# Kernel optimization log

Measured on AMD Instinct MI355X. Metric: run time of the kernel, lower is better.

## Reference

```python
import jax, jax.numpy as jnp
import numpy as np
import math

B, S, H, NH, HD, RD, INNER, MAXPOS, EPS = 2, 2048, 4096, 16, 256, 64, 16384, 2048, 1e-5


def setup_inputs() -> dict:
    key = jax.random.key(0)
    ks = jax.random.split(key, 8)
    sd = 0.02
    return {
        "hidden_states": jax.random.normal(ks[0], (B, S, H), jnp.float32),
        "attention_mask": jnp.ones((B, S), jnp.int32),
        "position_ids": jnp.broadcast_to(jnp.arange(S, dtype=jnp.int32), (B, S)),
        "ln_scale": jnp.ones((H,), jnp.float32),
        "ln_bias": jnp.zeros((H,), jnp.float32),
        "wq": jax.random.normal(ks[1], (H, H), jnp.float32) * sd,
        "wk": jax.random.normal(ks[2], (H, H), jnp.float32) * sd,
        "wv": jax.random.normal(ks[3], (H, H), jnp.float32) * sd,
        "wo": jax.random.normal(ks[4], (H, H), jnp.float32) * sd,
        "w_in": jax.random.normal(ks[5], (H, INNER), jnp.float32) * sd,
        "b_in": jnp.zeros((INNER,), jnp.float32),
        "w_out": jax.random.normal(ks[6], (INNER, H), jnp.float32) * sd,
        "b_out": jnp.zeros((H,), jnp.float32),
    }


def _rotate_every_two(t):
    # interleave (-odd, even) pairs along last dim
    r = jnp.stack((-t[..., 1::2], t[..., ::2]), axis=-1)
    return r.reshape(t.shape)


def reference(hidden_states, attention_mask, position_ids, ln_scale, ln_bias,
              wq, wk, wv, wo, w_in, b_in, w_out, b_out):
    x = hidden_states
    # LayerNorm (single ln feeds both attn and mlp in GPT-J parallel block)
    mu = jnp.mean(x, axis=-1, keepdims=True)
    var = jnp.mean(jnp.square(x - mu), axis=-1, keepdims=True)
    h = (x - mu) * jax.lax.rsqrt(var + EPS) * ln_scale + ln_bias

    # QKV projections (no bias), split heads: [B,S,NH,HD]
    q = (h @ wq).reshape(B, S, NH, HD)
    k = (h @ wk).reshape(B, S, NH, HD)
    v = (h @ wv).reshape(B, S, NH, HD)

    # sinusoidal table over rotary_dim, gathered by position_ids
    pos = jnp.arange(MAXPOS, dtype=jnp.float32)
    inv_freq = 1.0 / (10000.0 ** (jnp.arange(0, RD, 2, dtype=jnp.float32) / RD))
    freqs = pos[:, None] * inv_freq[None, :]          # [MAXPOS, RD//2]
    table = jnp.concatenate([jnp.sin(freqs), jnp.cos(freqs)], axis=-1)  # [MAXPOS, RD]
    sincos = table[position_ids]                      # [B,S,RD]
    sin, cos = jnp.split(sincos, 2, axis=-1)          # each [B,S,RD//2]
    sinr = jnp.repeat(sin[:, :, None, :], 2, axis=3)  # [B,S,1,RD]
    cosr = jnp.repeat(cos[:, :, None, :], 2, axis=3)

    def rope(t):
        return t * cosr + _rotate_every_two(t) * sinr

    q = jnp.concatenate([rope(q[..., :RD]), q[..., RD:]], axis=-1)
    k = jnp.concatenate([rope(k[..., :RD]), k[..., RD:]], axis=-1)

    # combined causal + padding mask -> additive bias
    causal = jnp.tril(jnp.ones((S, S), dtype=bool))
    mask = (attention_mask[:, None, None, :] > 0) & causal[None, None, :, :]
    bias = jnp.where(mask, 0.0, jnp.finfo(jnp.float32).min)  # [B,1,S,S]

    scale = 1.0 / math.sqrt(HD)
    scores = jnp.einsum('bqhd,bkhd->bhqk', q, k) * scale + bias
    attn = jax.nn.softmax(scores, axis=-1)
    ctx = jnp.einsum('bhqk,bkhd->bqhd', attn, v).reshape(B, S, H)
    attn_out = ctx @ wo

    # MLP on the same LN output (parallel residual), gelu_new ~ tanh gelu
    mlp = jax.nn.gelu(h @ w_in + b_in, approximate=True) @ w_out + b_out

    return x + attn_out + mlp
```

## Files before the change

### kernel.cpp

```cpp
#include <hip/hip_runtime.h>
#include <hip/hip_bf16.h>
#include <math.h>

namespace {

constexpr int kB = 2;
constexpr int kS = 2048;
constexpr int kH = 4096;
constexpr int kNH = 16;
constexpr int kHD = 256;

typedef __attribute__((ext_vector_type(4))) float f32x4;
typedef __attribute__((ext_vector_type(8))) short bf16x8;

__device__ __forceinline__ unsigned short f2bf(float f) {
  unsigned int u = __float_as_uint(f);
  u += 0x7FFFu + ((u >> 16) & 1u);
  return (unsigned short)(u >> 16);
}
__device__ __forceinline__ float bf2f(unsigned short h) {
  return __uint_as_float(((unsigned int)h) << 16);
}
__device__ __forceinline__ void gl2lds16(const void* g, void* l) {
  __builtin_amdgcn_global_load_lds(
      (const __attribute__((address_space(1))) unsigned int*)g,
      (__attribute__((address_space(3))) unsigned int*)l, 16, 0, 0);
}

#define SBAR asm volatile("s_barrier" ::: "memory")
#define LGKM0 asm volatile("s_waitcnt lgkmcnt(0)" ::: "memory")

__global__ __launch_bounds__(256) void ln_fwd(
    const float* __restrict__ x, const float* __restrict__ gam,
    const float* __restrict__ bet, unsigned short* __restrict__ hout,
    float* __restrict__ outp) {
  int row = blockIdx.x;
  int t = threadIdx.x;
  const float4* xr = (const float4*)(x + (size_t)row * kH);
  float4 v[4];
  float sum = 0.f, sq = 0.f;
#pragma unroll
  for (int i = 0; i < 4; i++) {
    v[i] = xr[t + i * 256];
    sum += v[i].x + v[i].y + v[i].z + v[i].w;
    sq += v[i].x * v[i].x + v[i].y * v[i].y + v[i].z * v[i].z + v[i].w * v[i].w;
  }
#pragma unroll
  for (int o = 32; o > 0; o >>= 1) {
    sum += __shfl_xor(sum, o);
    sq += __shfl_xor(sq, o);
  }
  __shared__ float red[8];
  if ((t & 63) == 0) { red[t >> 6] = sum; red[4 + (t >> 6)] = sq; }
  __syncthreads();
  sum = red[0] + red[1] + red[2] + red[3];
  sq = red[4] + red[5] + red[6] + red[7];
  float mu = sum * (1.f / kH);
  float rstd = rsqrtf(sq * (1.f / kH) - mu * mu + 1e-5f);
  const float4* gp = (const float4*)gam;
  const float4* bp = (const float4*)bet;
  ushort4* hr = (ushort4*)(hout + (size_t)row * kH);
  float4* orow = (float4*)(outp + (size_t)row * kH);
#pragma unroll
  for (int i = 0; i < 4; i++) {
    float4 g = gp[t + i * 256];
    float4 bb = bp[t + i * 256];
    ushort4 hv;
    hv.x = f2bf((v[i].x - mu) * rstd * g.x + bb.x);
    hv.y = f2bf((v[i].y - mu) * rstd * g.y + bb.y);
    hv.z = f2bf((v[i].z - mu) * rstd * g.z + bb.z);
    hv.w = f2bf((v[i].w - mu) * rstd * g.w + bb.w);
    hr[t + i * 256] = hv;
    orow[t + i * 256] = v[i];
  }
}

__global__ __launch_bounds__(256) void cvt_t(
    const float* __restrict__ in, int ldin, unsigned short* __restrict__ outp,
    int ldout) {
  __shared__ float tile[32][33];
  int n0 = blockIdx.x * 32, k0 = blockIdx.y * 32;
  int tx = threadIdx.x, ty = threadIdx.y;
#pragma unroll
  for (int i = 0; i < 4; i++)
    tile[ty + i * 8][tx] = in[(size_t)(k0 + ty + i * 8) * ldin + n0 + tx];
  __syncthreads();
#pragma unroll
  for (int i = 0; i < 4; i++)
    outp[(size_t)(n0 + ty + i * 8) * ldout + k0 + tx] =
        f2bf(tile[tx][ty + i * 8]);
}

__global__ __launch_bounds__(256) void vtrans(
    const unsigned short* __restrict__ v, unsigned short* __restrict__ vt) {
  __shared__ unsigned short tile[32][33];
  int bh = blockIdx.z;
  int s0 = blockIdx.x * 32, d0 = blockIdx.y * 32;
  int tx = threadIdx.x, ty = threadIdx.y;
  int b = bh >> 4, h = bh & 15;
  const unsigned short* src = v + (size_t)(b * kS) * kH + h * kHD;
#pragma unroll
  for (int i = 0; i < 4; i++)
    tile[ty + i * 8][tx] = src[(size_t)(s0 + ty + i * 8) * kH + d0 + tx];
  __syncthreads();
  unsigned short* dst = vt + (size_t)bh * kHD * kS;
#pragma unroll
  for (int i = 0; i < 4; i++)
    dst[(size_t)(d0 + ty + i * 8) * kS + s0 + tx] = tile[tx][ty + i * 8];
}

__global__ __launch_bounds__(256) void rope_scale(
    unsigned short* __restrict__ q, unsigned short* __restrict__ k,
    const int* __restrict__ pos) {
  int idx = blockIdx.x * 256 + threadIdx.x;
  int j = idx & 127;
  int rowh = idx >> 7;
  int h = rowh & 15;
  int s = (rowh >> 4) & 2047;
  int b = rowh >> 15;
  size_t off = ((size_t)(b * kS + s)) * kH + h * kHD + 2 * j;
  const float SCALE = 0.0625f;
  if (j < 32) {
    int p = pos[b * kS + s];
    float inv = exp2f(-(float)j * (13.287712379549449f / 32.f));
    float fr = (float)p * inv;
    float sn, cs;
    sincosf(fr, &sn, &cs);
    float e = bf2f(q[off]), o = bf2f(q[off + 1]);
    q[off] = f2bf((e * cs - o * sn) * SCALE);
    q[off + 1] = f2bf((o * cs + e * sn) * SCALE);
    e = bf2f(k[off]); o = bf2f(k[off + 1]);
    k[off] = f2bf(e * cs - o * sn);
    k[off + 1] = f2bf(o * cs + e * sn);
  } else {
    q[off] = f2bf(bf2f(q[off]) * SCALE);
    q[off + 1] = f2bf(bf2f(q[off + 1]) * SCALE);
  }
}

template <int EPI>
__global__ __launch_bounds__(512, 4) void gemmk(
    const unsigned short* __restrict__ A, int lda,
    const unsigned short* __restrict__ Bt, int ldb, void* __restrict__ Cp,
    int ldc, const float* __restrict__ bias, int K, int gx) {
  __shared__ __align__(16) char lds[73728];
  const int t = threadIdx.x;
  const int lane = t & 63, w = t >> 6;
  const int wm = w >> 1, wn = w & 1;
  const int l15 = lane & 15, l4 = lane >> 4;

  const int nwg = gridDim.x;
  const int orig = blockIdx.x;
  const int wg = (orig & 7) * (nwg >> 3) + (orig >> 3);
  const int bx = wg % gx, by = wg / gx;
  const int m0 = by * 256, n0 = bx * 128;

  const int lr = t >> 2, ch = t & 3;
  const int swo = ((ch ^ ((lr & 3) ^ ((lr >> 2) & 3))) << 3);
  const unsigned short* aS0 = A + (size_t)(m0 + lr) * lda + swo;
  const unsigned short* aS1 = A + (size_t)(m0 + 128 + lr) * lda + swo;
  const unsigned short* bS = Bt + (size_t)(n0 + lr) * ldb + swo;
  const int t16 = t * 16;

  const int keyR = (l15 & 3) ^ ((l15 >> 2) & 3);
  const int rch = ((l4 ^ keyR) << 4);
  const int abase = wm * 4096 + l15 * 64 + rch;
  const int bbase = 16384 + wn * 4096 + l15 * 64 + rch;

  f32x4 acc[4][4];
#pragma unroll
  for (int m = 0; m < 4; m++)
#pragma unroll
    for (int n = 0; n < 4; n++) acc[m][n] = (f32x4)(0.f);

  gl2lds16(aS0, lds + t16);
  gl2lds16(aS1, lds + 8192 + t16);
  gl2lds16(bS, lds + 16384 + t16);
  aS0 += 32; aS1 += 32; bS += 32;
  gl2lds16(aS0, lds + 24576 + t16);
  gl2lds16(aS1, lds + 24576 + 8192 + t16);
  gl2lds16(bS, lds + 24576 + 16384 + t16);
  aS0 += 32; aS1 += 32; bS += 32;
  asm volatile("s_waitcnt vmcnt(3)" ::: "memory");
  SBAR;

  int offR = 0, off1 = 24576, offW = 49152;
  const int nt = K >> 5;
  for (int kt = 0; kt < nt; ++kt) {
    if (kt + 2 < nt) {
      gl2lds16(aS0, lds + offW + t16);
      gl2lds16(aS1, lds + offW + 8192 + t16);
      gl2lds16(bS, lds + offW + 16384 + t16);
      aS0 += 32; aS1 += 32; bS += 32;
    }
    const char* cur = lds + offR;
    bf16x8 af[4], bv[4];
#pragma unroll
    for (int m = 0; m < 4; m++)
      af[m] = *(const bf16x8*)(cur + abase + m * 1024);
#pragma unroll
    for (int n = 0; n < 4; n++)
      bv[n] = *(const bf16x8*)(cur + bbase + n * 1024);
    __builtin_amdgcn_s_setprio(1);
#pragma unroll
    for (int m = 0; m < 4; m++)
#pragma unroll
      for (int n = 0; n < 4; n++)
        acc[m][n] = __builtin_amdgcn_mfma_f32_16x16x32_bf16(af[m], bv[n],
                                                            acc[m][n], 0, 0, 0);
    __builtin_amdgcn_s_setprio(0);
    LGKM0;
    if (kt + 2 < nt) asm volatile("s_waitcnt vmcnt(3)" ::: "memory");
    else             asm volatile("s_waitcnt vmcnt(0)" ::: "memory");
    SBAR;
    int tmp = offR; offR = off1; off1 = offW; offW = tmp;
  }

  const int crow = m0 + wm * 64 + l4 * 4;
  const int ccol = n0 + wn * 64 + l15;
#pragma unroll
  for (int m = 0; m < 4; m++) {
#pragma unroll
    for (int n = 0; n < 4; n++) {
      int col = ccol + n * 16;
#pragma unroll
      for (int r = 0; r < 4; r++) {
        int row = crow + m * 16 + r;
        float v = acc[m][n][r];
        size_t idx = (size_t)row * ldc + col;
        if constexpr (EPI == 0) {
          ((unsigned short*)Cp)[idx] = f2bf(v);
        } else if constexpr (EPI == 1) {
          float u = v + bias[col];
          float c = 0.7978845608028654f * (u + 0.044715f * u * u * u);
          float g = u / (1.0f + __expf(-2.0f * c));
          ((unsigned short*)Cp)[idx] = f2bf(g);
        } else if constexpr (EPI == 2) {
          ((float*)Cp)[idx] += v;
        } else {
          ((float*)Cp)[idx] += v + bias[col];
        }
      }
    }
  }
}

__global__ __launch_bounds__(512) void attn_fwd(
    const unsigned short* __restrict__ q, const unsigned short* __restrict__ k,
    const unsigned short* __restrict__ vt, const int* __restrict__ amask,
    unsigned short* __restrict__ ctx) {
  __shared__ __align__(16) char alds[147456];
  const int t = threadIdx.x, lane = t & 63, w = t >> 6;
  const int bid = blockIdx.x;
  const int qb = 15 - (bid >> 5);
  const int bh = bid & 31;
  const int b = bh >> 4, h = bh & 15;
  const int l15 = lane & 15, l4 = lane >> 4;
  const int qbase = qb * 128;

  bf16x8 qf[8];
  {
    int qrow = qbase + w * 16 + l15;
    const unsigned short* qp =
        q + (size_t)(b * kS + qrow) * kH + h * kHD + l4 * 8;
#pragma unroll
    for (int ks = 0; ks < 8; ks++) qf[ks] = *(const bf16x8*)(qp + ks * 32);
  }
  f32x4 o[16];
#pragma unroll
  for (int nf = 0; nf < 16; nf++) o[nf] = (f32x4)(0.f);
  float mr[4] = {-INFINITY, -INFINITY, -INFINITY, -INFINITY};
  float lr[4] = {0.f, 0.f, 0.f, 0.f};

  const unsigned short* kbase = k + (size_t)(b * kS) * kH + h * kHD;
  const unsigned short* vbase = vt + (size_t)bh * kHD * kS;
  unsigned short* sPw = (unsigned short*)(alds + 131072 + w * 2048);
  const int nt = 2 * qb + 2;

  const int krow = t >> 5, kch = t & 31;
  const int kcs = (kch ^ (krow & 7)) * 8;
  const int vrow = t >> 3, vch = t & 7;
  const int vcs = (vch ^ (vrow & 7)) * 8;
  const int t16b = t * 16;

#define ATTN_STAGE(KV0, BUF)                                                 \
  {                                                                          \
    char* kd = alds + (BUF) * 32768;                                         \
    char* vd = alds + 65536 + (BUF) * 32768;                                 \
    _Pragma("unroll") for (int i = 0; i < 4; i++) {                          \
      gl2lds16(kbase + (size_t)((KV0) + krow + i * 16) * kH + kcs,           \
               kd + i * 8192 + t16b);                                        \
      gl2lds16(vbase + (size_t)(vrow + i * 64) * kS + (KV0) + vcs,           \
               vd + i * 8192 + t16b);                                        \
    }                                                                        \
  }

  ATTN_STAGE(0, 0)

  for (int kvt = 0; kvt < nt; kvt++) {
    const int kv0 = kvt * 64;
    const int cb = kvt & 1;
    if (kvt + 1 < nt) {
      ATTN_STAGE(kv0 + 64, cb ^ 1)
      asm volatile("s_waitcnt vmcnt(8)" ::: "memory");
    } else {
      asm volatile("s_waitcnt vmcnt(0)" ::: "memory");
    }
    asm volatile("s_barrier" ::: "memory");

    const unsigned short* sK = (const unsigned short*)(alds + cb * 32768);
    const unsigned short* sV =
        (const unsigned short*)(alds + 65536 + cb * 32768);

    f32x4 sc[4];
#pragma unroll
    for (int g = 0; g < 4; g++) sc[g] = (f32x4)(0.f);
    __builtin_amdgcn_s_setprio(1);
#pragma unroll
    for (int g = 0; g < 4; g++) {
      int row = g * 16 + l15;
#pragma unroll
      for (int ks = 0; ks < 8; ks++) {
        bf16x8 kf =
            *(const bf16x8*)&sK[row * 256 + (((ks * 4 + l4) ^ (row & 7)) * 8)];
        sc[g] = __builtin_amdgcn_mfma_f32_16x16x32_bf16(qf[ks], kf, sc[g], 0, 0, 0);
      }
    }
    __builtin_amdgcn_s_setprio(0);

    int am[4];
#pragma unroll
    for (int g = 0; g < 4; g++) am[g] = amask[b * kS + kv0 + g * 16 + l15];
    float mx[4];
#pragma unroll
    for (int r = 0; r < 4; r++) {
      int qi = qbase + w * 16 + l4 * 4 + r;
      float a = -INFINITY;
#pragma unroll
      for (int g = 0; g < 4; g++) {
        bool ok = (kv0 + g * 16 + l15 <= qi) && (am[g] != 0);
        float s = ok ? sc[g][r] : -INFINITY;
        sc[g][r] = s;
        a = fmaxf(a, s);
      }
#pragma unroll
      for (int d = 1; d < 16; d <<= 1) a = fmaxf(a, __shfl_xor(a, d));
      mx[r] = a;
    }
    bool nd = false;
#pragma unroll
    for (int r = 0; r < 4; r++) nd |= (mx[r] > mr[r] + 8.f);
    if (__any(nd)) {
#pragma unroll
      for (int r = 0; r < 4; r++) {
        float nm = fmaxf(mr[r], mx[r]);
        float c = __expf(mr[r] - nm);
        lr[r] *= c;
        mr[r] = nm;
#pragma unroll
        for (int nf = 0; nf < 16; nf++) o[nf][r] *= c;
      }
    }
#pragma unroll
    for (int r = 0; r < 4; r++) {
      int prow = l4 * 4 + r;
      int pkey = (prow ^ (prow >> 2)) & 7;
      float rs = 0.f;
#pragma unroll
      for (int g = 0; g < 4; g++) {
        float p = __expf(sc[g][r] - mr[r]);
        rs += p;
        int kvl = g * 16 + l15;
        sPw[prow * 64 + (((kvl >> 3) ^ pkey) << 3) + (kvl & 7)] = f2bf(p);
      }
#pragma unroll
      for (int d = 1; d < 16; d <<= 1) rs += __shfl_xor(rs, d);
      lr[r] += rs;
    }
    asm volatile("s_waitcnt lgkmcnt(0)" ::: "memory");

    int rkey = (l15 ^ (l15 >> 2)) & 7;
    bf16x8 pa[2];
#pragma unroll
    for (int ks2 = 0; ks2 < 2; ks2++)
      pa[ks2] = *(const bf16x8*)&sPw[l15 * 64 + (((ks2 * 4 + l4) ^ rkey) << 3)];
    __builtin_amdgcn_s_setprio(1);
#pragma unroll
    for (int nf = 0; nf < 16; nf++) {
      int vr = nf * 16 + l15;
#pragma unroll
      for (int ks2 = 0; ks2 < 2; ks2++) {
        bf16x8 vf =
            *(const bf16x8*)&sV[vr * 64 + (((ks2 * 4 + l4) ^ (vr & 7)) * 8)];
        o[nf] = __builtin_amdgcn_mfma_f32_16x16x32_bf16(pa[ks2], vf, o[nf], 0, 0, 0);
      }
    }
    __builtin_amdgcn_s_setprio(0);
    asm volatile("s_barrier" ::: "memory");
  }

  float invl[4];
#pragma unroll
  for (int r = 0; r < 4; r++) invl[r] = 1.0f / lr[r];
#pragma unroll
  for (int nf = 0; nf < 16; nf++) {
    int d = nf * 16 + l15;
#pragma unroll
    for (int r = 0; r < 4; r++) {
      int qi = qbase + w * 16 + l4 * 4 + r;
      ctx[(size_t)(b * kS + qi) * kH + h * kHD + d] = f2bf(o[nf][r] * invl[r]);
    }
  }
#undef ATTN_STAGE
}

}

extern "C" void kernel_launch(void* const* d_in, const int* in_sizes, int n_in,
                              void* d_out, int out_size, void* d_ws,
                              size_t ws_size, hipStream_t stream) {
  const float* x = (const float*)d_in[0];
  const int* amask = (const int*)d_in[1];
  const int* pos = (const int*)d_in[2];
  const float* lns = (const float*)d_in[3];
  const float* lnb = (const float*)d_in[4];
  const float* wq = (const float*)d_in[5];
  const float* wk = (const float*)d_in[6];
  const float* wv = (const float*)d_in[7];
  const float* wo = (const float*)d_in[8];
  const float* w_in = (const float*)d_in[9];
  const float* b_in = (const float*)d_in[10];
  const float* w_out = (const float*)d_in[11];
  const float* b_out = (const float*)d_in[12];
  float* out = (float*)d_out;

  if (ws_size < 268435456ull) return;
  char* ws = (char*)d_ws;
  unsigned short* h_bf = (unsigned short*)ws;
  unsigned short* big = (unsigned short*)(ws + 33554432ull);
  unsigned short* vbuf = (unsigned short*)(ws + 167772160ull);
  unsigned short* wbuf = (unsigned short*)(ws + 201326592ull);
  unsigned short* mid = big;
  unsigned short* qbuf = big;
  unsigned short* kbuf = big + 16777216;
  unsigned short* vtb = big + 33554432;
  unsigned short* ctxb = vbuf;

  dim3 t256(256);
  dim3 t512(512);
  dim3 t32x8(32, 8);

  ln_fwd<<<kB * kS, t256, 0, stream>>>(x, lns, lnb, h_bf, out);

  for (int c = 0; c < 2; c++) {
    cvt_t<<<dim3(256, 128), t32x8, 0, stream>>>(w_in + c * 8192, 16384, wbuf, 4096);
    gemmk<1><<<dim3(1024), t512, 0, stream>>>(
        h_bf, 4096, wbuf, 4096, mid + c * 8192, 16384, b_in + c * 8192, 4096, 64);
  }
  for (int c = 0; c < 2; c++) {
    cvt_t<<<dim3(128, 256), t32x8, 0, stream>>>(
        w_out + (size_t)c * 8192 * 4096, 4096, wbuf, 8192);
    if (c == 0)
      gemmk<3><<<dim3(512), t512, 0, stream>>>(mid + c * 8192, 16384, wbuf,
                                               8192, out, 4096, b_out, 8192, 32);
    else
      gemmk<2><<<dim3(512), t512, 0, stream>>>(
          mid + c * 8192, 16384, wbuf, 8192, out, 4096, nullptr, 8192, 32);
  }

  const float* wqkv[3] = {wq, wk, wv};
  unsigned short* qkvp[3] = {qbuf, kbuf, vbuf};
  for (int i = 0; i < 3; i++) {
    cvt_t<<<dim3(128, 128), t32x8, 0, stream>>>(wqkv[i], 4096, wbuf, 4096);
    gemmk<0><<<dim3(512), t512, 0, stream>>>(h_bf, 4096, wbuf, 4096,
                                             qkvp[i], 4096, nullptr, 4096, 32);
  }
  rope_scale<<<32768, t256, 0, stream>>>(qbuf, kbuf, pos);
  vtrans<<<dim3(64, 8, 32), t32x8, 0, stream>>>(vbuf, vtb);
  attn_fwd<<<dim3(512), t512, 0, stream>>>(qbuf, kbuf, vtb, amask, ctxb);
  cvt_t<<<dim3(128, 128), t32x8, 0, stream>>>(wo, 4096, wbuf, 4096);
  gemmk<2><<<dim3(512), t512, 0, stream>>>(ctxb, 4096, wbuf, 4096, out,
                                           4096, nullptr, 4096, 32);
}
```

Measured before the change: 2.342 ms.

## Replace GEMM with 256x256-tile kernel using LDS flag sync and 4-stage ring

Swaps the 256x128-tile, triple-buffered GEMM for a 256x256-tile kernel. Each of its 8 waves computes an 8x4 grid of MFMA tiles. Workgroup s_barriers are replaced by per-wave progress flags in LDS: waves spin with s_sleep until every wave has finished loading the current k-slice, over a 4-slot LDS ring with a new swizzle. The aim is more data reuse per tile and less barrier stall. The cost is doubled accumulator registers, lower occupancy (launch bounds 2), and spin-wait overhead and ordering risk.

```diff
diff --git a/kernel.cpp b/kernel.cpp
--- a/kernel.cpp
+++ b/kernel.cpp
@@ -26,9 +26,6 @@
       (const __attribute__((address_space(1))) unsigned int*)g,
       (__attribute__((address_space(3))) unsigned int*)l, 16, 0, 0);
 }
-
-#define SBAR asm volatile("s_barrier" ::: "memory")
-#define LGKM0 asm volatile("s_waitcnt lgkmcnt(0)" ::: "memory")
 
 __global__ __launch_bounds__(256) void ln_fwd(
     const float* __restrict__ x, const float* __restrict__ gam,
@@ -139,87 +136,103 @@
 }
 
 template <int EPI>
-__global__ __launch_bounds__(512, 4) void gemmk(
+__global__ __launch_bounds__(512, 2) void gemmpc(
     const unsigned short* __restrict__ A, int lda,
     const unsigned short* __restrict__ Bt, int ldb, void* __restrict__ Cp,
     int ldc, const float* __restrict__ bias, int K, int gx) {
-  __shared__ __align__(16) char lds[73728];
+  __shared__ __align__(16) char lds[131072 + 32];
+  volatile unsigned* fl = (volatile unsigned*)(lds + 131072);
   const int t = threadIdx.x;
   const int lane = t & 63, w = t >> 6;
-  const int wm = w >> 1, wn = w & 1;
+  const int wm = w >> 2, wn = w & 3;
   const int l15 = lane & 15, l4 = lane >> 4;
 
   const int nwg = gridDim.x;
   const int orig = blockIdx.x;
   const int wg = (orig & 7) * (nwg >> 3) + (orig >> 3);
   const int bx = wg % gx, by = wg / gx;
-  const int m0 = by * 256, n0 = bx * 128;
-
-  const int lr = t >> 2, ch = t & 3;
-  const int swo = ((ch ^ ((lr & 3) ^ ((lr >> 2) & 3))) << 3);
-  const unsigned short* aS0 = A + (size_t)(m0 + lr) * lda + swo;
-  const unsigned short* aS1 = A + (size_t)(m0 + 128 + lr) * lda + swo;
-  const unsigned short* bS = Bt + (size_t)(n0 + lr) * ldb + swo;
-  const int t16 = t * 16;
-
-  const int keyR = (l15 & 3) ^ ((l15 >> 2) & 3);
-  const int rch = ((l4 ^ keyR) << 4);
-  const int abase = wm * 4096 + l15 * 64 + rch;
-  const int bbase = 16384 + wn * 4096 + l15 * 64 + rch;
-
-  f32x4 acc[4][4];
-#pragma unroll
-  for (int m = 0; m < 4; m++)
+  const int m0 = by * 256, n0 = bx * 256;
+
+  const unsigned short* sp[4];
+#pragma unroll
+  for (int i = 0; i < 4; i++) {
+    int g = w * 256 + i * 64 + lane;
+    int gin = g & 1023;
+    int p = gin >> 3, s = (gin & 7) ^ (p & 7);
+    int row = 2 * p + (s >> 2), chunk = s & 3;
+    sp[i] = (g < 1024 ? A + (size_t)(m0 + row) * lda
+                      : Bt + (size_t)(n0 + row) * ldb) + chunk * 8;
+  }
+  const int dstoff = w * 4096 + lane * 16;
+
+  const int swz = ((((l15 & 1) << 2) | l4) ^ ((l15 >> 1) & 7)) << 4;
+  const int abase = wm * 8192 + ((l15 >> 1) << 7) + swz;
+  const int bbase = 16384 + wn * 4096 + ((l15 >> 1) << 7) + swz;
+
+  f32x4 acc[8][4];
+#pragma unroll
+  for (int m = 0; m < 8; m++)
 #pragma unroll
     for (int n = 0; n < 4; n++) acc[m][n] = (f32x4)(0.f);
 
-  gl2lds16(aS0, lds + t16);
-  gl2lds16(aS1, lds + 8192 + t16);
-  gl2lds16(bS, lds + 16384 + t16);
-  aS0 += 32; aS1 += 32; bS += 32;
-  gl2lds16(aS0, lds + 24576 + t16);
-  gl2lds16(aS1, lds + 24576 + 8192 + t16);
-  gl2lds16(bS, lds + 24576 + 16384 + t16);
-  aS0 += 32; aS1 += 32; bS += 32;
-  asm volatile("s_waitcnt vmcnt(3)" ::: "memory");
-  SBAR;
-
-  int offR = 0, off1 = 24576, offW = 49152;
+  if (lane == 0) fl[w] = 0;
+  __syncthreads();
+  {
+    char* dst = lds + dstoff;
+#pragma unroll
+    for (int i = 0; i < 4; i++) gl2lds16(sp[i], dst + i * 1024);
+#pragma unroll
+    for (int i = 0; i < 4; i++) sp[i] += 32;
+  }
+
   const int nt = K >> 5;
   for (int kt = 0; kt < nt; ++kt) {
-    if (kt + 2 < nt) {
-      gl2lds16(aS0, lds + offW + t16);
-      gl2lds16(aS1, lds + offW + 8192 + t16);
-      gl2lds16(bS, lds + offW + 16384 + t16);
-      aS0 += 32; aS1 += 32; bS += 32;
-    }
-    const char* cur = lds + offR;
-    bf16x8 af[4], bv[4];
-#pragma unroll
-    for (int m = 0; m < 4; m++)
+    if (kt + 1 < nt) {
+      char* dst = lds + ((kt + 1) & 3) * 32768 + dstoff;
+#pragma unroll
+      for (int i = 0; i < 4; i++) gl2lds16(sp[i], dst + i * 1024);
+#pragma unroll
+      for (int i = 0; i < 4; i++) sp[i] += 32;
+      asm volatile("s_waitcnt vmcnt(4)" ::: "memory");
+    } else {
+      asm volatile("s_waitcnt vmcnt(0)" ::: "memory");
+    }
+    if (lane == 0) fl[w] = (unsigned)(kt + 1);
+    {
+      int spins = 0;
+      while (spins < (1 << 22)) {
+        unsigned v = fl[lane & 7];
+        v = min(v, (unsigned)__shfl_xor((int)v, 1));
+        v = min(v, (unsigned)__shfl_xor((int)v, 2));
+        v = min(v, (unsigned)__shfl_xor((int)v, 4));
+        if (v >= (unsigned)(kt + 1)) break;
+        __builtin_amdgcn_s_sleep(1);
+        ++spins;
+      }
+    }
+    __builtin_amdgcn_sched_barrier(0);
+    const char* cur = lds + (kt & 3) * 32768;
+    bf16x8 af[8], bv[4];
+#pragma unroll
+    for (int m = 0; m < 8; m++)
       af[m] = *(const bf16x8*)(cur + abase + m * 1024);
 #pragma unroll
     for (int n = 0; n < 4; n++)
       bv[n] = *(const bf16x8*)(cur + bbase + n * 1024);
     __builtin_amdgcn_s_setprio(1);
 #pragma unroll
-    for (int m = 0; m < 4; m++)
+    for (int m = 0; m < 8; m++)
 #pragma unroll
       for (int n = 0; n < 4; n++)
         acc[m][n] = __builtin_amdgcn_mfma_f32_16x16x32_bf16(af[m], bv[n],
                                                             acc[m][n], 0, 0, 0);
     __builtin_amdgcn_s_setprio(0);
-    LGKM0;
-    if (kt + 2 < nt) asm volatile("s_waitcnt vmcnt(3)" ::: "memory");
-    else             asm volatile("s_waitcnt vmcnt(0)" ::: "memory");
-    SBAR;
-    int tmp = offR; offR = off1; off1 = offW; offW = tmp;
-  }
-
-  const int crow = m0 + wm * 64 + l4 * 4;
+  }
+
+  const int crow = m0 + wm * 128 + l4 * 4;
   const int ccol = n0 + wn * 64 + l15;
 #pragma unroll
-  for (int m = 0; m < 4; m++) {
+  for (int m = 0; m < 8; m++) {
 #pragma unroll
     for (int n = 0; n < 4; n++) {
       int col = ccol + n * 16;
@@ -454,31 +467,31 @@
 
   for (int c = 0; c < 2; c++) {
     cvt_t<<<dim3(256, 128), t32x8, 0, stream>>>(w_in + c * 8192, 16384, wbuf, 4096);
-    gemmk<1><<<dim3(1024), t512, 0, stream>>>(
-        h_bf, 4096, wbuf, 4096, mid + c * 8192, 16384, b_in + c * 8192, 4096, 64);
+    gemmpc<1><<<dim3(512), t512, 0, stream>>>(
+        h_bf, 4096, wbuf, 4096, mid + c * 8192, 16384, b_in + c * 8192, 4096, 32);
   }
   for (int c = 0; c < 2; c++) {
     cvt_t<<<dim3(128, 256), t32x8, 0, stream>>>(
         w_out + (size_t)c * 8192 * 4096, 4096, wbuf, 8192);
     if (c == 0)
-      gemmk<3><<<dim3(512), t512, 0, stream>>>(mid + c * 8192, 16384, wbuf,
-                                               8192, out, 4096, b_out, 8192, 32);
+      gemmpc<3><<<dim3(256), t512, 0, stream>>>(mid + c * 8192, 16384, wbuf,
+                                                8192, out, 4096, b_out, 8192, 16);
     else
-      gemmk<2><<<dim3(512), t512, 0, stream>>>(
-          mid + c * 8192, 16384, wbuf, 8192, out, 4096, nullptr, 8192, 32);
+      gemmpc<2><<<dim3(256), t512, 0, stream>>>(
+          mid + c * 8192, 16384, wbuf, 8192, out, 4096, nullptr, 8192, 16);
   }
 
   const float* wqkv[3] = {wq, wk, wv};
   unsigned short* qkvp[3] = {qbuf, kbuf, vbuf};
   for (int i = 0; i < 3; i++) {
     cvt_t<<<dim3(128, 128), t32x8, 0, stream>>>(wqkv[i], 4096, wbuf, 4096);
-    gemmk<0><<<dim3(512), t512, 0, stream>>>(h_bf, 4096, wbuf, 4096,
-                                             qkvp[i], 4096, nullptr, 4096, 32);
+    gemmpc<0><<<dim3(256), t512, 0, stream>>>(h_bf, 4096, wbuf, 4096,
+                                              qkvp[i], 4096, nullptr, 4096, 16);
   }
   rope_scale<<<32768, t256, 0, stream>>>(qbuf, kbuf, pos);
   vtrans<<<dim3(64, 8, 32), t32x8, 0, stream>>>(vbuf, vtb);
   attn_fwd<<<dim3(512), t512, 0, stream>>>(qbuf, kbuf, vtb, amask, ctxb);
   cvt_t<<<dim3(128, 128), t32x8, 0, stream>>>(wo, 4096, wbuf, 4096);
-  gemmk<2><<<dim3(512), t512, 0, stream>>>(ctxb, 4096, wbuf, 4096, out,
-                                           4096, nullptr, 4096, 32);
-}
+  gemmpc<2><<<dim3(256), t512, 0, stream>>>(ctxb, 4096, wbuf, 4096, out,
+                                            4096, nullptr, 4096, 16);
+}
```

Measured after the change: 2.533 ms. +8.1%, slower.
